# Kernel tuning notes

Hardware: AMD Instinct MI355X
Metric: run time of the kernel (lower is better)

Reference implementation:

```python
import jax, jax.numpy as jnp
import numpy as np

EPS = 1e-8

def setup_inputs() -> dict:
    key = jax.random.key(0)
    k0, k1, k2, k3, k4 = jax.random.split(key, 5)
    B, N, K, Q, L, F = 8, 5, 5, 4, 128, 768
    support_emb = jax.random.normal(k0, (B, N, K, L, F), dtype=jnp.float32)
    query_emb = jax.random.normal(k1, (B, N * Q, L, F), dtype=jnp.float32)
    B_mask = jax.random.randint(k2, (B, N, K, L), 0, 2, dtype=jnp.int32)
    I_mask = jax.random.randint(k3, (B, N, K, L), 0, 2, dtype=jnp.int32)
    trigger_label = jax.random.randint(k4, (B, N * Q, L), 0, 2 * N + 1, dtype=jnp.int32)
    return {"support_emb": support_emb, "query_emb": query_emb, "B_mask": B_mask,
            "I_mask": I_mask, "trigger_label": trigger_label, "N": N, "K": K, "Q": Q}

def _proto(support_emb, Bm, Im, N):
    # support_emb: (B,N,K,L,F); Bm/Im: (B,N,K,L) float
    sum_B = jnp.einsum('bnklf,bnkl->bnf', support_emb, Bm)
    cnt_B = Bm.sum((2, 3))[..., None] + EPS
    pB = sum_B / cnt_B                                   # (B,N,F)
    sum_I = jnp.einsum('bnklf,bnkl->bnf', support_emb, Im)
    cnt_I = Im.sum((2, 3))[..., None] + EPS
    pI = sum_I / cnt_I                                   # (B,N,F)
    Om = 1.0 - Bm - Im                                   # (B,N,K,L)
    sum_O = jnp.einsum('bnklf,bnkl->bf', support_emb, Om)
    cnt_O = Om.sum((1, 2, 3))[:, None] + EPS
    pO = sum_O / cnt_O                                   # (B,F)
    Bsz, F = pO.shape
    # interleave: tags [O, B_0, I_0, B_1, I_1, ...]
    pBI = jnp.stack([pB, pI], axis=2).reshape(Bsz, 2 * N, F)
    return jnp.concatenate([pO[:, None, :], pBI], axis=1)  # (B, 2N+1, F)

def reference(support_emb, query_emb, B_mask, I_mask, trigger_label, N, K, Q):
    dt = support_emb.dtype
    Bm = B_mask.astype(dt)
    Im = I_mask.astype(dt)
    prototype = _proto(support_emb, Bm, Im, N)             # (B, 2N+1, F)
    # similarity: broadcast dot product -> batched GEMM
    logits = jnp.einsum('bqlf,btf->bqlt', query_emb, prototype)  # (B, NQ, L, 2N+1)
    T = logits.shape[-1]
    flat = logits.reshape(-1, T)
    pred = jnp.argmax(flat, axis=1)
    lab = trigger_label.reshape(-1)
    logp = jax.nn.log_softmax(flat, axis=-1)
    loss = -jnp.take_along_axis(logp, lab[:, None], axis=1).mean()
    return (loss, logits, pred)
```

## Files before the change

### kernel.cpp

```cpp
#include <hip/hip_runtime.h>
#include <cstdint>
#include <cstddef>

#define EPS 1e-8f

#define Bsz 8
#define Nn  5
#define Kk  5
#define Qq  4
#define Ll  128
#define Ff  768
#define NQ  (Nn*Qq)
#define Tt  (2*Nn+1)
#define KL  (Kk*Ll)
#define ROWS_PER_B (NQ*Ll)
#define NROWS (Bsz*ROWS_PER_B)
#define F4  (Ff/4)
#define BN  (Bsz*Nn)

#define S1_CHUNK 32
#define S1_CH    (KL / S1_CHUNK)

__global__ __launch_bounds__(256) void stage1_partials(
    const float* __restrict__ sup,
    const int*   __restrict__ Bm,
    const int*   __restrict__ Im,
    float* __restrict__ accum,
    float* __restrict__ cnt)
{
    int blk  = blockIdx.x;
    int bn   = blk / S1_CH;
    int ch   = blk - bn * S1_CH;
    int pos0 = ch * S1_CHUNK;
    int tid  = threadIdx.x;

    const float* sp = sup + ((size_t)bn * KL + pos0) * Ff;
    const int*   bp = Bm + bn * KL + pos0;
    const int*   ip = Im + bn * KL + pos0;

    __shared__ float smB[S1_CHUNK];
    __shared__ float smI[S1_CHUNK];
    if (tid < S1_CHUNK) {
        smB[tid] = (float)bp[tid];
        smI[tid] = (float)ip[tid];
    }
    __syncthreads();

    float aB0=0,aB1=0,aB2=0, aI0=0,aI1=0,aI2=0, aO0=0,aO1=0,aO2=0;
    const float* r = sp + tid;
    #pragma unroll 4
    for (int p = 0; p < S1_CHUNK; ++p, r += Ff) {
        float mb = smB[p], mi = smI[p];
        float mo = 1.0f - mb - mi;
        float v0 = r[0], v1 = r[256], v2 = r[512];
        aB0 = fmaf(mb, v0, aB0); aB1 = fmaf(mb, v1, aB1); aB2 = fmaf(mb, v2, aB2);
        aI0 = fmaf(mi, v0, aI0); aI1 = fmaf(mi, v1, aI1); aI2 = fmaf(mi, v2, aI2);
        aO0 = fmaf(mo, v0, aO0); aO1 = fmaf(mo, v1, aO1); aO2 = fmaf(mo, v2, aO2);
    }
    float* o = accum + (size_t)bn * (3 * Ff);
    atomicAdd(&o[tid],            aB0); atomicAdd(&o[tid + 256],          aB1); atomicAdd(&o[tid + 512],          aB2);
    atomicAdd(&o[Ff + tid],       aI0); atomicAdd(&o[Ff + tid + 256],     aI1); atomicAdd(&o[Ff + tid + 512],     aI2);
    atomicAdd(&o[2*Ff + tid],     aO0); atomicAdd(&o[2*Ff + tid + 256],   aO1); atomicAdd(&o[2*Ff + tid + 512],   aO2);

    if (tid == 0) { float c = 0; for (int p = 0; p < S1_CHUNK; ++p) c += smB[p]; atomicAdd(&cnt[bn*2],   c); }
    if (tid == 1) { float c = 0; for (int p = 0; p < S1_CHUNK; ++p) c += smI[p]; atomicAdd(&cnt[bn*2+1], c); }
}

__global__ void stage2_proto(
    const float* __restrict__ accum,
    const float* __restrict__ cnt,
    float* __restrict__ proto)
{
    int b = blockIdx.x;
    int f = threadIdx.x;

    float sumO = 0.0f, cntO = 0.0f;
    #pragma unroll
    for (int n = 0; n < Nn; ++n) {
        int bn = b * Nn + n;
        const float* a = accum + (size_t)bn * (3 * Ff);
        float cB = cnt[bn*2], cI = cnt[bn*2+1];
        proto[((size_t)b * Tt + (1 + 2 * n)) * Ff + f] = a[f]        / (cB + EPS);
        proto[((size_t)b * Tt + (2 + 2 * n)) * Ff + f] = a[Ff + f]   / (cI + EPS);
        sumO += a[2*Ff + f];
        cntO += (float)KL - cB - cI;
    }
    proto[(size_t)b * Tt * Ff + f] = sumO / (cntO + EPS);
}

#define S3_BLOCKS_PER_B 160
#define S3_ROWS_PER_WAVE 4

__global__ __launch_bounds__(256) void stage3_logits(
    const float* __restrict__ query,
    const float* __restrict__ proto,
    const int*   __restrict__ label,
    float* __restrict__ out_logits,
    float* __restrict__ out_pred,
    float* __restrict__ loss_out)
{
    __shared__ float sLoss;

    int b  = blockIdx.x / S3_BLOCKS_PER_B;
    int rg = blockIdx.x - b * S3_BLOCKS_PER_B;
    int wave = threadIdx.x >> 6;
    int lane = threadIdx.x & 63;

    if (threadIdx.x == 0) sLoss = 0.0f;
    __syncthreads();

    const float4* pg = (const float4*)(proto + (size_t)b * Tt * Ff);
    float4 P[Tt][3];
    #pragma unroll
    for (int t = 0; t < Tt; ++t) {
        P[t][0] = pg[t * F4 + lane];
        P[t][1] = pg[t * F4 + 64 + lane];
        P[t][2] = pg[t * F4 + 128 + lane];
    }

    int row0 = rg * (4 * S3_ROWS_PER_WAVE) + wave * S3_ROWS_PER_WAVE;
    float wloss = 0.0f;

    for (int r = 0; r < S3_ROWS_PER_WAVE; ++r) {
        size_t grow = (size_t)b * ROWS_PER_B + row0 + r;
        const float4* q = (const float4*)(query + grow * Ff);
        float4 q0 = q[lane], q1 = q[64 + lane], q2 = q[128 + lane];
        int lab = label[grow];

        float acc[Tt];
        #pragma unroll
        for (int t = 0; t < Tt; ++t) {
            float d;
            d = q0.x * P[t][0].x;
            d = fmaf(q0.y, P[t][0].y, d); d = fmaf(q0.z, P[t][0].z, d); d = fmaf(q0.w, P[t][0].w, d);
            d = fmaf(q1.x, P[t][1].x, d); d = fmaf(q1.y, P[t][1].y, d);
            d = fmaf(q1.z, P[t][1].z, d); d = fmaf(q1.w, P[t][1].w, d);
            d = fmaf(q2.x, P[t][2].x, d); d = fmaf(q2.y, P[t][2].y, d);
            d = fmaf(q2.z, P[t][2].z, d); d = fmaf(q2.w, P[t][2].w, d);
            acc[t] = d;
        }
        #pragma unroll
        for (int off = 32; off > 0; off >>= 1) {
            #pragma unroll
            for (int t = 0; t < Tt; ++t) acc[t] += __shfl_xor(acc[t], off, 64);
        }
        float m = acc[0]; int bt = 0;
        #pragma unroll
        for (int t = 1; t < Tt; ++t) if (acc[t] > m) { m = acc[t]; bt = t; }
        float s = 0.0f;
        #pragma unroll
        for (int t = 0; t < Tt; ++t) s += __expf(acc[t] - m);
        float labv = acc[0];
        #pragma unroll
        for (int t = 1; t < Tt; ++t) labv = (lab == t) ? acc[t] : labv;
        float myv = acc[0];
        #pragma unroll
        for (int t = 1; t < Tt; ++t) myv = (lane == t) ? acc[t] : myv;

        if (lane < Tt) out_logits[grow * Tt + lane] = myv;
        if (lane == 0) out_pred[grow] = (float)bt;
        wloss += (m + __logf(s)) - labv;
    }

    if (lane == 0) atomicAdd(&sLoss, wloss);
    __syncthreads();
    if (threadIdx.x == 0) atomicAdd(loss_out, sLoss * (1.0f / (float)NROWS));
}

extern "C" void kernel_launch(void* const* d_in, const int* in_sizes, int n_in,
                              void* d_out, int out_size, void* d_ws, size_t ws_size,
                              hipStream_t stream) {
    const float* sup   = (const float*)d_in[0];
    const float* query = (const float*)d_in[1];
    const int*   Bm    = (const int*)d_in[2];
    const int*   Im    = (const int*)d_in[3];
    const int*   lab   = (const int*)d_in[4];

    float* w     = (float*)d_ws;
    float* accum = w;
    float* cnt   = accum + (size_t)BN * 3 * Ff;
    float* proto = cnt + 2 * BN;
    size_t zeroBytes = ((size_t)BN * 3 * Ff + 2 * BN) * sizeof(float);

    float* loss_out   = (float*)d_out;
    float* out_logits = (float*)d_out + 1;
    float* out_pred   = (float*)d_out + 1 + (size_t)NROWS * Tt;

    hipMemsetAsync(d_ws, 0, zeroBytes, stream);
    hipMemsetAsync(d_out, 0, sizeof(float), stream);

    stage1_partials<<<BN * S1_CH, 256, 0, stream>>>(sup, Bm, Im, accum, cnt);
    stage2_proto<<<Bsz, Ff, 0, stream>>>(accum, cnt, proto);
    stage3_logits<<<Bsz * S3_BLOCKS_PER_B, 256, 0, stream>>>(query, proto, lab,
                                                             out_logits, out_pred, loss_out);
}
```

Baseline: 208.8 us.

## Rewrite all stages: per-block partials, parallel reduce, LDS-tiled two-row logits

Stage 1 now writes per-block float4 partial sums instead of issuing global atomics, with smaller row chunks and 192-thread blocks. Stage 2 becomes a wide parallel reduction over those partials rather than an 8-block kernel. Stage 3 stages the prototypes in padded LDS and has each group of four lanes compute two query rows, cutting the cross-lane shuffles to two steps. The workspace memset shrinks to just the counts. In exchange, stage 1 writes a larger partial buffer and the loss is reduced through one atomic per wave.

```diff
diff --git a/kernel.cpp b/kernel.cpp
--- a/kernel.cpp
+++ b/kernel.cpp
@@ -7,91 +7,119 @@
 #define Bsz 8
 #define Nn  5
 #define Kk  5
-#define Qq  4
 #define Ll  128
 #define Ff  768
-#define NQ  (Nn*Qq)
-#define Tt  (2*Nn+1)
-#define KL  (Kk*Ll)
-#define ROWS_PER_B (NQ*Ll)
-#define NROWS (Bsz*ROWS_PER_B)
-#define F4  (Ff/4)
-#define BN  (Bsz*Nn)
-
-#define S1_CHUNK 32
-#define S1_CH    (KL / S1_CHUNK)
-
-__global__ __launch_bounds__(256) void stage1_partials(
+#define Tt  11
+#define KL  640
+#define ROWS_PER_B 2560
+#define NROWS 20480
+#define F4  192
+#define BN  40
+
+#define S1_ROWS 16
+#define S1_CH   (KL / S1_ROWS)
+#define S1_NBLK (BN * S1_CH)
+#define PART_STRIDE (3 * Ff)
+#define PART_STRIDE4 (PART_STRIDE / 4)
+
+__global__ __launch_bounds__(192) void stage1(
     const float* __restrict__ sup,
     const int*   __restrict__ Bm,
     const int*   __restrict__ Im,
-    float* __restrict__ accum,
+    float* __restrict__ part,
     float* __restrict__ cnt)
 {
-    int blk  = blockIdx.x;
-    int bn   = blk / S1_CH;
-    int ch   = blk - bn * S1_CH;
-    int pos0 = ch * S1_CHUNK;
-    int tid  = threadIdx.x;
-
-    const float* sp = sup + ((size_t)bn * KL + pos0) * Ff;
-    const int*   bp = Bm + bn * KL + pos0;
-    const int*   ip = Im + bn * KL + pos0;
-
-    __shared__ float smB[S1_CHUNK];
-    __shared__ float smI[S1_CHUNK];
-    if (tid < S1_CHUNK) {
+    int blk = blockIdx.x;
+    int bn  = blk / S1_CH;
+    int ch  = blk - bn * S1_CH;
+    int tid = threadIdx.x;
+
+    const float4* sp = (const float4*)(sup + ((size_t)bn * KL + ch * S1_ROWS) * Ff);
+    const int*    bp = Bm + bn * KL + ch * S1_ROWS;
+    const int*    ip = Im + bn * KL + ch * S1_ROWS;
+
+    __shared__ float smB[S1_ROWS];
+    __shared__ float smI[S1_ROWS];
+    if (tid < S1_ROWS) {
         smB[tid] = (float)bp[tid];
         smI[tid] = (float)ip[tid];
     }
     __syncthreads();
 
-    float aB0=0,aB1=0,aB2=0, aI0=0,aI1=0,aI2=0, aO0=0,aO1=0,aO2=0;
-    const float* r = sp + tid;
-    #pragma unroll 4
-    for (int p = 0; p < S1_CHUNK; ++p, r += Ff) {
+    float4 aB = {0,0,0,0}, aI = {0,0,0,0}, aO = {0,0,0,0};
+    #pragma unroll 8
+    for (int p = 0; p < S1_ROWS; ++p) {
+        float4 v = sp[tid + p * F4];
         float mb = smB[p], mi = smI[p];
         float mo = 1.0f - mb - mi;
-        float v0 = r[0], v1 = r[256], v2 = r[512];
-        aB0 = fmaf(mb, v0, aB0); aB1 = fmaf(mb, v1, aB1); aB2 = fmaf(mb, v2, aB2);
-        aI0 = fmaf(mi, v0, aI0); aI1 = fmaf(mi, v1, aI1); aI2 = fmaf(mi, v2, aI2);
-        aO0 = fmaf(mo, v0, aO0); aO1 = fmaf(mo, v1, aO1); aO2 = fmaf(mo, v2, aO2);
-    }
-    float* o = accum + (size_t)bn * (3 * Ff);
-    atomicAdd(&o[tid],            aB0); atomicAdd(&o[tid + 256],          aB1); atomicAdd(&o[tid + 512],          aB2);
-    atomicAdd(&o[Ff + tid],       aI0); atomicAdd(&o[Ff + tid + 256],     aI1); atomicAdd(&o[Ff + tid + 512],     aI2);
-    atomicAdd(&o[2*Ff + tid],     aO0); atomicAdd(&o[2*Ff + tid + 256],   aO1); atomicAdd(&o[2*Ff + tid + 512],   aO2);
-
-    if (tid == 0) { float c = 0; for (int p = 0; p < S1_CHUNK; ++p) c += smB[p]; atomicAdd(&cnt[bn*2],   c); }
-    if (tid == 1) { float c = 0; for (int p = 0; p < S1_CHUNK; ++p) c += smI[p]; atomicAdd(&cnt[bn*2+1], c); }
-}
-
-__global__ void stage2_proto(
-    const float* __restrict__ accum,
+        aB.x = fmaf(mb, v.x, aB.x); aB.y = fmaf(mb, v.y, aB.y);
+        aB.z = fmaf(mb, v.z, aB.z); aB.w = fmaf(mb, v.w, aB.w);
+        aI.x = fmaf(mi, v.x, aI.x); aI.y = fmaf(mi, v.y, aI.y);
+        aI.z = fmaf(mi, v.z, aI.z); aI.w = fmaf(mi, v.w, aI.w);
+        aO.x = fmaf(mo, v.x, aO.x); aO.y = fmaf(mo, v.y, aO.y);
+        aO.z = fmaf(mo, v.z, aO.z); aO.w = fmaf(mo, v.w, aO.w);
+    }
+    float4* o = (float4*)(part + (size_t)blk * PART_STRIDE);
+    o[tid]          = aB;
+    o[F4 + tid]     = aI;
+    o[2 * F4 + tid] = aO;
+
+    if (tid == 0) { float s = 0; for (int p = 0; p < S1_ROWS; ++p) s += smB[p]; atomicAdd(&cnt[2*bn],   s); }
+    if (tid == 1) { float s = 0; for (int p = 0; p < S1_ROWS; ++p) s += smI[p]; atomicAdd(&cnt[2*bn+1], s); }
+}
+
+__global__ __launch_bounds__(256) void stage2(
+    const float* __restrict__ part,
     const float* __restrict__ cnt,
     float* __restrict__ proto)
 {
-    int b = blockIdx.x;
-    int f = threadIdx.x;
-
-    float sumO = 0.0f, cntO = 0.0f;
-    #pragma unroll
-    for (int n = 0; n < Nn; ++n) {
-        int bn = b * Nn + n;
-        const float* a = accum + (size_t)bn * (3 * Ff);
-        float cB = cnt[bn*2], cI = cnt[bn*2+1];
-        proto[((size_t)b * Tt + (1 + 2 * n)) * Ff + f] = a[f]        / (cB + EPS);
-        proto[((size_t)b * Tt + (2 + 2 * n)) * Ff + f] = a[Ff + f]   / (cI + EPS);
-        sumO += a[2*Ff + f];
-        cntO += (float)KL - cB - cI;
-    }
-    proto[(size_t)b * Tt * Ff + f] = sumO / (cntO + EPS);
-}
-
-#define S3_BLOCKS_PER_B 160
-#define S3_ROWS_PER_WAVE 4
-
-__global__ __launch_bounds__(256) void stage3_logits(
+    int gid = blockIdx.x * 256 + threadIdx.x;
+    float4* protoP4 = (float4*)proto;
+
+    if (gid < BN * 2 * F4) {
+        int bn  = gid / (2 * F4);
+        int r   = gid - bn * 2 * F4;
+        int set = r / F4;
+        int f4  = r - set * F4;
+        const float4* src = (const float4*)(part + (size_t)bn * S1_CH * PART_STRIDE + set * Ff) + f4;
+        float4 s = {0,0,0,0};
+        #pragma unroll 8
+        for (int c = 0; c < S1_CH; ++c) {
+            float4 v = src[(size_t)c * PART_STRIDE4];
+            s.x += v.x; s.y += v.y; s.z += v.z; s.w += v.w;
+        }
+        float sc = 1.0f / (cnt[2 * bn + set] + EPS);
+        int b = bn / Nn, n = bn - b * Nn;
+        int tag = 1 + 2 * n + set;
+        float4 o = { s.x * sc, s.y * sc, s.z * sc, s.w * sc };
+        protoP4[((size_t)b * Tt + tag) * F4 + f4] = o;
+    } else if (gid < BN * 2 * F4 + Bsz * F4) {
+        int idx = gid - BN * 2 * F4;
+        int b   = idx / F4;
+        int f4  = idx - b * F4;
+        float4 s = {0,0,0,0};
+        float cO = (float)(KL * Nn);
+        for (int n = 0; n < Nn; ++n) {
+            int bn = b * Nn + n;
+            const float4* src = (const float4*)(part + (size_t)bn * S1_CH * PART_STRIDE + 2 * Ff) + f4;
+            #pragma unroll 8
+            for (int c = 0; c < S1_CH; ++c) {
+                float4 v = src[(size_t)c * PART_STRIDE4];
+                s.x += v.x; s.y += v.y; s.z += v.z; s.w += v.w;
+            }
+            cO -= cnt[2 * bn] + cnt[2 * bn + 1];
+        }
+        float sc = 1.0f / (cO + EPS);
+        float4 o = { s.x * sc, s.y * sc, s.z * sc, s.w * sc };
+        protoP4[(size_t)b * Tt * F4 + f4] = o;
+    }
+}
+
+#define S3_ROWS 64
+#define S3_NBLK (NROWS / S3_ROWS)
+#define BLKS_PER_B (ROWS_PER_B / S3_ROWS)
+
+__global__ __launch_bounds__(128) void stage3(
     const float* __restrict__ query,
     const float* __restrict__ proto,
     const int*   __restrict__ label,
@@ -99,72 +127,82 @@
     float* __restrict__ out_pred,
     float* __restrict__ loss_out)
 {
-    __shared__ float sLoss;
-
-    int b  = blockIdx.x / S3_BLOCKS_PER_B;
-    int rg = blockIdx.x - b * S3_BLOCKS_PER_B;
-    int wave = threadIdx.x >> 6;
+    __shared__ float4 ldsP[Tt * 4 * 49];
+
+    int blk = blockIdx.x;
+    int b   = blk / BLKS_PER_B;
+
+    const float4* pg = (const float4*)(proto + (size_t)b * Tt * Ff);
+    for (int idx = threadIdx.x; idx < Tt * F4; idx += 128) {
+        int t  = idx / F4;
+        int f4 = idx - t * F4;
+        int s  = f4 / 48;
+        int j  = f4 - 48 * s;
+        ldsP[(t * 4 + s) * 49 + j] = pg[idx];
+    }
+    __syncthreads();
+
+    int w    = threadIdx.x >> 6;
     int lane = threadIdx.x & 63;
-
-    if (threadIdx.x == 0) sLoss = 0.0f;
-    __syncthreads();
-
-    const float4* pg = (const float4*)(proto + (size_t)b * Tt * Ff);
-    float4 P[Tt][3];
+    int p    = lane >> 2;
+    int s    = lane & 3;
+
+    size_t row0 = (size_t)blk * S3_ROWS + w * 32 + p * 2;
+    const float4* q0 = (const float4*)(query + row0 * Ff) + s * 48;
+    const float4* q1 = q0 + F4;
+
+    float a0[Tt], a1[Tt];
+    #pragma unroll
+    for (int t = 0; t < Tt; ++t) { a0[t] = 0.0f; a1[t] = 0.0f; }
+
+    const float4* pb = &ldsP[s * 49];
+    #pragma unroll 2
+    for (int j = 0; j < 48; ++j) {
+        float4 u = q0[j];
+        float4 v = q1[j];
+        #pragma unroll
+        for (int t = 0; t < Tt; ++t) {
+            float4 pv = pb[t * (4 * 49) + j];
+            float d0 = a0[t], d1 = a1[t];
+            d0 = fmaf(u.x, pv.x, d0); d0 = fmaf(u.y, pv.y, d0);
+            d0 = fmaf(u.z, pv.z, d0); d0 = fmaf(u.w, pv.w, d0);
+            d1 = fmaf(v.x, pv.x, d1); d1 = fmaf(v.y, pv.y, d1);
+            d1 = fmaf(v.z, pv.z, d1); d1 = fmaf(v.w, pv.w, d1);
+            a0[t] = d0; a1[t] = d1;
+        }
+    }
+
     #pragma unroll
     for (int t = 0; t < Tt; ++t) {
-        P[t][0] = pg[t * F4 + lane];
-        P[t][1] = pg[t * F4 + 64 + lane];
-        P[t][2] = pg[t * F4 + 128 + lane];
-    }
-
-    int row0 = rg * (4 * S3_ROWS_PER_WAVE) + wave * S3_ROWS_PER_WAVE;
+        a0[t] += __shfl_xor(a0[t], 1, 64); a0[t] += __shfl_xor(a0[t], 2, 64);
+        a1[t] += __shfl_xor(a1[t], 1, 64); a1[t] += __shfl_xor(a1[t], 2, 64);
+    }
+
     float wloss = 0.0f;
-
-    for (int r = 0; r < S3_ROWS_PER_WAVE; ++r) {
-        size_t grow = (size_t)b * ROWS_PER_B + row0 + r;
-        const float4* q = (const float4*)(query + grow * Ff);
-        float4 q0 = q[lane], q1 = q[64 + lane], q2 = q[128 + lane];
-        int lab = label[grow];
-
-        float acc[Tt];
+    if (s == 0) {
         #pragma unroll
-        for (int t = 0; t < Tt; ++t) {
-            float d;
-            d = q0.x * P[t][0].x;
-            d = fmaf(q0.y, P[t][0].y, d); d = fmaf(q0.z, P[t][0].z, d); d = fmaf(q0.w, P[t][0].w, d);
-            d = fmaf(q1.x, P[t][1].x, d); d = fmaf(q1.y, P[t][1].y, d);
-            d = fmaf(q1.z, P[t][1].z, d); d = fmaf(q1.w, P[t][1].w, d);
-            d = fmaf(q2.x, P[t][2].x, d); d = fmaf(q2.y, P[t][2].y, d);
-            d = fmaf(q2.z, P[t][2].z, d); d = fmaf(q2.w, P[t][2].w, d);
-            acc[t] = d;
-        }
-        #pragma unroll
-        for (int off = 32; off > 0; off >>= 1) {
-            #pragma unroll
-            for (int t = 0; t < Tt; ++t) acc[t] += __shfl_xor(acc[t], off, 64);
-        }
-        float m = acc[0]; int bt = 0;
-        #pragma unroll
-        for (int t = 1; t < Tt; ++t) if (acc[t] > m) { m = acc[t]; bt = t; }
-        float s = 0.0f;
-        #pragma unroll
-        for (int t = 0; t < Tt; ++t) s += __expf(acc[t] - m);
-        float labv = acc[0];
-        #pragma unroll
-        for (int t = 1; t < Tt; ++t) labv = (lab == t) ? acc[t] : labv;
-        float myv = acc[0];
-        #pragma unroll
-        for (int t = 1; t < Tt; ++t) myv = (lane == t) ? acc[t] : myv;
-
-        if (lane < Tt) out_logits[grow * Tt + lane] = myv;
-        if (lane == 0) out_pred[grow] = (float)bt;
-        wloss += (m + __logf(s)) - labv;
-    }
-
-    if (lane == 0) atomicAdd(&sLoss, wloss);
-    __syncthreads();
-    if (threadIdx.x == 0) atomicAdd(loss_out, sLoss * (1.0f / (float)NROWS));
+        for (int rr = 0; rr < 2; ++rr) {
+            size_t grow = row0 + rr;
+            float* a = rr ? a1 : a0;
+            float m = a[0]; int bt = 0;
+            #pragma unroll
+            for (int t = 1; t < Tt; ++t) if (a[t] > m) { m = a[t]; bt = t; }
+            float sum = 0.0f;
+            #pragma unroll
+            for (int t = 0; t < Tt; ++t) sum += __expf(a[t] - m);
+            int lab = label[grow];
+            float labv = a[0];
+            #pragma unroll
+            for (int t = 1; t < Tt; ++t) labv = (lab == t) ? a[t] : labv;
+            #pragma unroll
+            for (int t = 0; t < Tt; ++t) out_logits[grow * Tt + t] = a[t];
+            out_pred[grow] = (float)bt;
+            wloss += (m + __logf(sum)) - labv;
+        }
+    }
+    #pragma unroll
+    for (int off = 32; off > 0; off >>= 1) wloss += __shfl_xor(wloss, off, 64);
+    if (lane == 0) atomicAdd(loss_out, wloss * (1.0f / (float)NROWS));
 }
 
 extern "C" void kernel_launch(void* const* d_in, const int* in_sizes, int n_in,
@@ -177,20 +215,18 @@
     const int*   lab   = (const int*)d_in[4];
 
     float* w     = (float*)d_ws;
-    float* accum = w;
-    float* cnt   = accum + (size_t)BN * 3 * Ff;
+    float* part  = w;
+    float* cnt   = part + (size_t)S1_NBLK * PART_STRIDE;
     float* proto = cnt + 2 * BN;
-    size_t zeroBytes = ((size_t)BN * 3 * Ff + 2 * BN) * sizeof(float);
 
     float* loss_out   = (float*)d_out;
     float* out_logits = (float*)d_out + 1;
     float* out_pred   = (float*)d_out + 1 + (size_t)NROWS * Tt;
 
-    hipMemsetAsync(d_ws, 0, zeroBytes, stream);
+    hipMemsetAsync(cnt, 0, 2 * BN * sizeof(float), stream);
     hipMemsetAsync(d_out, 0, sizeof(float), stream);
 
-    stage1_partials<<<BN * S1_CH, 256, 0, stream>>>(sup, Bm, Im, accum, cnt);
-    stage2_proto<<<Bsz, Ff, 0, stream>>>(accum, cnt, proto);
-    stage3_logits<<<Bsz * S3_BLOCKS_PER_B, 256, 0, stream>>>(query, proto, lab,
-                                                             out_logits, out_pred, loss_out);
-}
+    stage1<<<S1_NBLK, 192, 0, stream>>>(sup, Bm, Im, part, cnt);
+    stage2<<<66, 256, 0, stream>>>(part, cnt, proto);
+    stage3<<<S3_NBLK, 128, 0, stream>>>(query, proto, lab, out_logits, out_pred, loss_out);
+}
```

Result: slower. 225.4 us (+8.0%).
